# Performance work log

Hardware: AMD Instinct MI355X
Metric: run time of the kernel (lower is better)

## Reference

```python
import jax, jax.numpy as jnp
import numpy as np
import itertools

N = 65536          # points
R = 1.0 / 16.0     # radius (forward uses 1/16)
K = 64             # max_num_neighbors in forward call
G = 16             # grid cells per axis (cell size == R)


def _radius_knn_edges(pts):
    """Grid-hashed radius search; per point keep nearest K within R (self-loop included),
    pad with self index so every point has exactly K edges (max-aggregation neutral)."""
    cells = np.minimum((pts / R).astype(np.int64), G - 1)
    cid = (cells[:, 0] * G + cells[:, 1]) * G + cells[:, 2]
    order = np.argsort(cid, kind='stable')
    sorted_cid = cid[order]
    counts = np.bincount(cid, minlength=G ** 3)
    starts = np.concatenate([[0], np.cumsum(counts)[:-1]])
    M = int(counts.max())
    cand = -np.ones((G ** 3, M), dtype=np.int64)
    slot = np.arange(N) - starts[sorted_cid]
    cand[sorted_cid, slot] = order
    offs = np.array(list(itertools.product([-1, 0, 1], repeat=3)))
    nbr = np.empty((N, K), dtype=np.int64)
    chunk = 4096
    for s in range(0, N, chunk):
        e = min(s + chunk, N)
        c = cells[s:e]
        nc = c[:, None, :] + offs[None]                      # [B,27,3]
        valid_c = np.all((nc >= 0) & (nc < G), axis=-1)      # [B,27]
        ncid = (nc[..., 0] * G + nc[..., 1]) * G + nc[..., 2]
        ncid = np.where(valid_c, ncid, 0)
        cd = cand[ncid]                                      # [B,27,M]
        cd = np.where(np.broadcast_to(valid_c[..., None], cd.shape), cd, -1)
        cd = cd.reshape(e - s, -1)                           # [B,27M]
        p = pts[np.maximum(cd, 0)]
        d = np.linalg.norm(p - pts[s:e, None, :], axis=-1)
        d = np.where((cd >= 0) & (d <= R), d, np.inf)
        sel = np.argsort(d, axis=1)[:, :K]
        row = np.arange(e - s)[:, None]
        picked = cd[row, sel]
        ok = np.isfinite(d[row, sel])
        nbr[s:e] = np.where(ok, picked, np.arange(s, e)[:, None])
    out_index = np.repeat(np.arange(N, dtype=np.int64), K)
    in_index = nbr.reshape(-1)
    return out_index, in_index


def setup_inputs() -> dict:
    key = jax.random.key(0)
    ks = jax.random.split(key, 16)
    pos = jax.random.uniform(ks[0], (N, 3), dtype=jnp.float32)
    rgb = jax.random.uniform(ks[1], (N, 3), dtype=jnp.float32)
    batch = jnp.zeros((N,), dtype=jnp.int64)
    oi, ii = _radius_knn_edges(np.asarray(pos, dtype=np.float64))
    out_index = jnp.asarray(oi)
    in_index = jnp.asarray(ii)

    def lin_w(k, fi, fo):
        return jax.random.normal(k, (fi, fo), dtype=jnp.float32) / np.sqrt(fi).astype(np.float32)

    def lin_b(k, fo):
        return 0.01 * jax.random.normal(k, (fo,), dtype=jnp.float32)

    return {
        'pos': pos, 'rgb': rgb, 'batch': batch,
        'out_index': out_index, 'in_index': in_index,
        'w1a': lin_w(ks[2], 6, 8),   'b1a': lin_b(ks[3], 8),
        'w1b': lin_w(ks[4], 8, 8),   'b1b': lin_b(ks[5], 8),
        'w2a': lin_w(ks[6], 11, 16), 'b2a': lin_b(ks[7], 16),
        'w2b': lin_w(ks[8], 16, 16), 'b2b': lin_b(ks[9], 16),
        'w3a': lin_w(ks[10], 19, 32), 'b3a': lin_b(ks[11], 32),
        'w3b': lin_w(ks[12], 32, 32), 'b3b': lin_b(ks[13], 32),
    }


def _point_conv(x, pos, out_index, in_index, wa, ba, wb, bb):
    # gather neighbor features + relative position, local MLP, max-scatter, output linear
    dpos = pos[in_index] - pos[out_index]                      # [E,3]
    msg = jnp.concatenate([x[in_index], dpos], axis=-1)        # [E,c_in+3]
    h = jax.nn.celu(msg @ wa + ba)                             # [E,c_mid]
    agg = jax.ops.segment_max(h, out_index, num_segments=pos.shape[0],
                              indices_are_sorted=True)         # [N,c_mid]
    return agg @ wb + bb                                       # [N,c_out]


def reference(pos, rgb, batch, out_index, in_index,
              w1a, b1a, w1b, b1b, w2a, b2a, w2b, b2b, w3a, b3a, w3b, b3b):
    out = jax.nn.celu(_point_conv(pos, pos, out_index, in_index, w1a, b1a, w1b, b1b))
    out = jax.nn.celu(_point_conv(out, pos, out_index, in_index, w2a, b2a, w2b, b2b))
    out = jax.nn.celu(_point_conv(out, pos, out_index, in_index, w3a, b3a, w3b, b3b))
    return (pos, out, batch)
```

## Files before the change

kernel.cpp:

```cpp
#include <hip/hip_runtime.h>
#include <hip/hip_fp16.h>
#include <math.h>


#define NPTS 65536
#define KNBR 64

__device__ __forceinline__ float celu1(float x) {
    return x > 0.0f ? x : (__expf(x) - 1.0f);
}

__device__ __forceinline__ unsigned pkmax(unsigned a, unsigned b) {
    unsigned d;
    asm("v_pk_max_f16 %0, %1, %2" : "=v"(d) : "v"(a), "v"(b));
    return d;
}

__device__ __forceinline__ unsigned pack2(float a, float b) {
    __half2 h = __floats2half2_rn(a, b);
    return *(unsigned*)&h;
}

__global__ __launch_bounds__(256) void k_prep(
    const float* __restrict__ pos,
    const float* __restrict__ w1a,
    const float* __restrict__ b1a,
    __half* __restrict__ q1,
    float* __restrict__ dout,
    int out_size)
{
    int t = blockIdx.x * 256 + threadIdx.x;
    if (t >= NPTS) return;
    float p0 = pos[3 * t + 0];
    float p1 = pos[3 * t + 1];
    float p2 = pos[3 * t + 2];
    dout[3 * t + 0] = p0;
    dout[3 * t + 1] = p1;
    dout[3 * t + 2] = p2;
    float q[8];
#pragma unroll
    for (int c = 0; c < 8; ++c) {
        float a = b1a[c];
        a = fmaf(p0, w1a[0 * 8 + c] + w1a[3 * 8 + c], a);
        a = fmaf(p1, w1a[1 * 8 + c] + w1a[4 * 8 + c], a);
        a = fmaf(p2, w1a[2 * 8 + c] + w1a[5 * 8 + c], a);
        q[c] = a;
    }
    uint4 pk;
    pk.x = pack2(q[0], q[1]);
    pk.y = pack2(q[2], q[3]);
    pk.z = pack2(q[4], q[5]);
    pk.w = pack2(q[6], q[7]);
    *(uint4*)(q1 + 8 * t) = pk;
    for (int j = 35 * NPTS + t; j < out_size; j += NPTS)
        dout[j] = 0.0f;
}

template <int FH, int FOUT, int FHN, bool WRITEX>
__global__ __launch_bounds__(256) void k_layer(
    const __half* __restrict__ q,
    const int* __restrict__ idx,
    const float* __restrict__ pos,
    const float* __restrict__ wap,
    const float* __restrict__ wb,
    const float* __restrict__ bb,
    const float* __restrict__ wan,
    const float* __restrict__ ban,
    float* __restrict__ xout,
    __half* __restrict__ qnext)
{
    constexpr int SL  = FH / 8;
    constexpr int LPP = SL * 8;
    constexpr int PPW = 64 / LPP;
    constexpr int NIT = 64 / (4 * PPW);

    __shared__ uint4 m_lds[64 * SL];

    int w  = threadIdx.x >> 6;
    int l  = threadIdx.x & 63;
    int pl = l / LPP;
    int u  = l % LPP;
    int c  = u % SL;
    int g  = u / SL;
    int pbase = blockIdx.x * 64;

#pragma unroll
    for (int it = 0; it < NIT; ++it) {
        int lp = it * (4 * PPW) + w * PPW + pl;
        int p  = pbase + lp;
        const uint4* ip = (const uint4*)(idx + p * KNBR + g * 8);
        uint4 i0 = ip[0];
        uint4 i1 = ip[1];
        uint4 v[8];
        v[0] = *(const uint4*)(q + (int)i0.x * FH + c * 8);
        v[1] = *(const uint4*)(q + (int)i0.y * FH + c * 8);
        v[2] = *(const uint4*)(q + (int)i0.z * FH + c * 8);
        v[3] = *(const uint4*)(q + (int)i0.w * FH + c * 8);
        v[4] = *(const uint4*)(q + (int)i1.x * FH + c * 8);
        v[5] = *(const uint4*)(q + (int)i1.y * FH + c * 8);
        v[6] = *(const uint4*)(q + (int)i1.z * FH + c * 8);
        v[7] = *(const uint4*)(q + (int)i1.w * FH + c * 8);

        unsigned ax = 0xFC00FC00u, ay = 0xFC00FC00u, az = 0xFC00FC00u, aw = 0xFC00FC00u;
#pragma unroll
        for (int k = 0; k < 8; ++k) {
            ax = pkmax(ax, v[k].x);
            ay = pkmax(ay, v[k].y);
            az = pkmax(az, v[k].z);
            aw = pkmax(aw, v[k].w);
        }
#pragma unroll
        for (int st = SL; st < LPP; st <<= 1) {
            ax = pkmax(ax, (unsigned)__shfl_xor((int)ax, st, 64));
            ay = pkmax(ay, (unsigned)__shfl_xor((int)ay, st, 64));
            az = pkmax(az, (unsigned)__shfl_xor((int)az, st, 64));
            aw = pkmax(aw, (unsigned)__shfl_xor((int)aw, st, 64));
        }
        if (g == 0) {
            uint4 r; r.x = ax; r.y = ay; r.z = az; r.w = aw;
            m_lds[lp * SL + c] = r;
        }
    }
    __syncthreads();

    if (threadIdx.x < 64) {
        int lt = threadIdx.x;
        int p  = pbase + lt;
        float p0 = pos[3 * p + 0];
        float p1 = pos[3 * p + 1];
        float p2 = pos[3 * p + 2];

        float h[FH];
#pragma unroll
        for (int s = 0; s < SL; ++s) {
            uint4 vv = m_lds[lt * SL + s];
            unsigned w4[4] = {vv.x, vv.y, vv.z, vv.w};
#pragma unroll
            for (int k = 0; k < 4; ++k) {
                float2 f = __half22float2(*(__half2*)&w4[k]);
                h[s * 8 + k * 2 + 0] = f.x;
                h[s * 8 + k * 2 + 1] = f.y;
            }
        }
#pragma unroll
        for (int ch = 0; ch < FH; ++ch) {
            float gg = p0 * wap[ch] + p1 * wap[FH + ch] + p2 * wap[2 * FH + ch];
            h[ch] = celu1(h[ch] - gg);
        }
        float x[FOUT];
#pragma unroll
        for (int c2 = 0; c2 < FOUT; ++c2) {
            float a = bb[c2];
#pragma unroll
            for (int ch = 0; ch < FH; ++ch)
                a = fmaf(h[ch], wb[ch * FOUT + c2], a);
            x[c2] = celu1(a);
        }
        if constexpr (WRITEX) {
            float4* xo = (float4*)(xout + (long long)p * FOUT);
#pragma unroll
            for (int c4 = 0; c4 < FOUT / 4; ++c4)
                xo[c4] = make_float4(x[4 * c4 + 0], x[4 * c4 + 1], x[4 * c4 + 2], x[4 * c4 + 3]);
        }
        if constexpr (FHN > 0) {
            float qn[FHN];
#pragma unroll
            for (int cn = 0; cn < FHN; ++cn) {
                float a = ban[cn];
#pragma unroll
                for (int c2 = 0; c2 < FOUT; ++c2)
                    a = fmaf(x[c2], wan[c2 * FHN + cn], a);
                a = fmaf(p0, wan[(FOUT + 0) * FHN + cn], a);
                a = fmaf(p1, wan[(FOUT + 1) * FHN + cn], a);
                a = fmaf(p2, wan[(FOUT + 2) * FHN + cn], a);
                qn[cn] = a;
            }
            uint4* qo = (uint4*)(qnext + p * FHN);
#pragma unroll
            for (int s = 0; s < FHN / 8; ++s) {
                uint4 pk;
                pk.x = pack2(qn[s * 8 + 0], qn[s * 8 + 1]);
                pk.y = pack2(qn[s * 8 + 2], qn[s * 8 + 3]);
                pk.z = pack2(qn[s * 8 + 4], qn[s * 8 + 5]);
                pk.w = pack2(qn[s * 8 + 6], qn[s * 8 + 7]);
                qo[s] = pk;
            }
        }
    }
}

extern "C" void kernel_launch(void* const* d_in, const int* in_sizes, int n_in,
                              void* d_out, int out_size, void* d_ws, size_t ws_size,
                              hipStream_t stream) {
    const float* pos = (const float*)d_in[0];
    const int* idx = (const int*)d_in[4];
    const float* w1a = (const float*)d_in[5];
    const float* b1a = (const float*)d_in[6];
    const float* w1b = (const float*)d_in[7];
    const float* b1b = (const float*)d_in[8];
    const float* w2a = (const float*)d_in[9];
    const float* b2a = (const float*)d_in[10];
    const float* w2b = (const float*)d_in[11];
    const float* b2b = (const float*)d_in[12];
    const float* w3a = (const float*)d_in[13];
    const float* b3a = (const float*)d_in[14];
    const float* w3b = (const float*)d_in[15];
    const float* b3b = (const float*)d_in[16];
    float* out = (float*)d_out;

    char* ws = (char*)d_ws;
    __half* A = (__half*)ws;
    __half* B = (__half*)(ws + (4u << 20));

    k_prep<<<NPTS / 256, 256, 0, stream>>>(pos, w1a, b1a, A, out, out_size);
    k_layer<8, 8, 16, false><<<NPTS / 64, 256, 0, stream>>>(
        A, idx, pos, w1a + 3 * 8, w1b, b1b, w2a, b2a, nullptr, B);
    k_layer<16, 16, 32, false><<<NPTS / 64, 256, 0, stream>>>(
        B, idx, pos, w2a + 8 * 16, w2b, b2b, w3a, b3a, nullptr, A);
    k_layer<32, 32, 0, true><<<NPTS / 64, 256, 0, stream>>>(
        A, idx, pos, w3a + 16 * 32, w3b, b3b, nullptr, nullptr, out + 3 * NPTS, nullptr);
}
```

Measured before the change: 177.0 us.

## Fuse prep and three layers into one cooperative persistent kernel with grid syncs

Merges the prep kernel and the three layer kernels into a single cooperative kernel that loops over tiles persistently and separates stages with grid-wide syncs, so the separate launches and the gaps between them go away. The final layer's output MLP is spread across all 256 threads (4 threads per point, 8 outputs each) instead of only 64. The next-layer projection is also computed in chunks of 8 to reduce register pressure. This adds grid-sync cost and a fixed grid of 1024 or 512 blocks, which may limit occupancy compared with the original many-block launches. A fallback to the old multi-kernel path remains.

```diff
diff --git a/kernel.cpp b/kernel.cpp
--- a/kernel.cpp
+++ b/kernel.cpp
@@ -1,10 +1,13 @@
 #include <hip/hip_runtime.h>
 #include <hip/hip_fp16.h>
+#include <hip/hip_cooperative_groups.h>
 #include <math.h>
 
 
 #define NPTS 65536
 #define KNBR 64
+
+namespace cg = cooperative_groups;
 
 __device__ __forceinline__ float celu1(float x) {
     return x > 0.0f ? x : (__expf(x) - 1.0f);
@@ -21,43 +24,9 @@
     return *(unsigned*)&h;
 }
 
-__global__ __launch_bounds__(256) void k_prep(
-    const float* __restrict__ pos,
-    const float* __restrict__ w1a,
-    const float* __restrict__ b1a,
-    __half* __restrict__ q1,
-    float* __restrict__ dout,
-    int out_size)
-{
-    int t = blockIdx.x * 256 + threadIdx.x;
-    if (t >= NPTS) return;
-    float p0 = pos[3 * t + 0];
-    float p1 = pos[3 * t + 1];
-    float p2 = pos[3 * t + 2];
-    dout[3 * t + 0] = p0;
-    dout[3 * t + 1] = p1;
-    dout[3 * t + 2] = p2;
-    float q[8];
-#pragma unroll
-    for (int c = 0; c < 8; ++c) {
-        float a = b1a[c];
-        a = fmaf(p0, w1a[0 * 8 + c] + w1a[3 * 8 + c], a);
-        a = fmaf(p1, w1a[1 * 8 + c] + w1a[4 * 8 + c], a);
-        a = fmaf(p2, w1a[2 * 8 + c] + w1a[5 * 8 + c], a);
-        q[c] = a;
-    }
-    uint4 pk;
-    pk.x = pack2(q[0], q[1]);
-    pk.y = pack2(q[2], q[3]);
-    pk.z = pack2(q[4], q[5]);
-    pk.w = pack2(q[6], q[7]);
-    *(uint4*)(q1 + 8 * t) = pk;
-    for (int j = 35 * NPTS + t; j < out_size; j += NPTS)
-        dout[j] = 0.0f;
-}
-
 template <int FH, int FOUT, int FHN, bool WRITEX>
-__global__ __launch_bounds__(256) void k_layer(
+__device__ __forceinline__ void layer_phase(
+    uint4* __restrict__ m_lds,
     const __half* __restrict__ q,
     const int* __restrict__ idx,
     const float* __restrict__ pos,
@@ -67,14 +36,13 @@
     const float* __restrict__ wan,
     const float* __restrict__ ban,
     float* __restrict__ xout,
-    __half* __restrict__ qnext)
+    __half* __restrict__ qnext,
+    int pbase)
 {
     constexpr int SL  = FH / 8;
     constexpr int LPP = SL * 8;
     constexpr int PPW = 64 / LPP;
     constexpr int NIT = 64 / (4 * PPW);
-
-    __shared__ uint4 m_lds[64 * SL];
 
     int w  = threadIdx.x >> 6;
     int l  = threadIdx.x & 63;
@@ -82,7 +50,6 @@
     int u  = l % LPP;
     int c  = u % SL;
     int g  = u / SL;
-    int pbase = blockIdx.x * 64;
 
 #pragma unroll
     for (int it = 0; it < NIT; ++it) {
@@ -123,7 +90,45 @@
     }
     __syncthreads();
 
-    if (threadIdx.x < 64) {
+    if constexpr (WRITEX) {
+        int pt  = threadIdx.x >> 2;
+        int qtr = threadIdx.x & 3;
+        int p   = pbase + pt;
+        float p0 = pos[3 * p + 0];
+        float p1 = pos[3 * p + 1];
+        float p2 = pos[3 * p + 2];
+
+        float h[FH];
+#pragma unroll
+        for (int s = 0; s < SL; ++s) {
+            uint4 vv = m_lds[pt * SL + s];
+            unsigned w4[4] = {vv.x, vv.y, vv.z, vv.w};
+#pragma unroll
+            for (int k = 0; k < 4; ++k) {
+                float2 f = __half22float2(*(__half2*)&w4[k]);
+                h[s * 8 + k * 2 + 0] = f.x;
+                h[s * 8 + k * 2 + 1] = f.y;
+            }
+        }
+#pragma unroll
+        for (int ch = 0; ch < FH; ++ch) {
+            float gg = p0 * wap[ch] + p1 * wap[FH + ch] + p2 * wap[2 * FH + ch];
+            h[ch] = celu1(h[ch] - gg);
+        }
+        float x[8];
+#pragma unroll
+        for (int j = 0; j < 8; ++j) {
+            int c2 = qtr * 8 + j;
+            float a = bb[c2];
+#pragma unroll
+            for (int ch = 0; ch < FH; ++ch)
+                a = fmaf(h[ch], wb[ch * FOUT + c2], a);
+            x[j] = celu1(a);
+        }
+        float4* xo = (float4*)(xout + (long long)p * FOUT + qtr * 8);
+        xo[0] = make_float4(x[0], x[1], x[2], x[3]);
+        xo[1] = make_float4(x[4], x[5], x[6], x[7]);
+    } else if (threadIdx.x < 64) {
         int lt = threadIdx.x;
         int p  = pbase + lt;
         float p0 = pos[3 * p + 0];
@@ -156,37 +161,129 @@
                 a = fmaf(h[ch], wb[ch * FOUT + c2], a);
             x[c2] = celu1(a);
         }
-        if constexpr (WRITEX) {
-            float4* xo = (float4*)(xout + (long long)p * FOUT);
-#pragma unroll
-            for (int c4 = 0; c4 < FOUT / 4; ++c4)
-                xo[c4] = make_float4(x[4 * c4 + 0], x[4 * c4 + 1], x[4 * c4 + 2], x[4 * c4 + 3]);
-        }
         if constexpr (FHN > 0) {
-            float qn[FHN];
-#pragma unroll
-            for (int cn = 0; cn < FHN; ++cn) {
-                float a = ban[cn];
-#pragma unroll
-                for (int c2 = 0; c2 < FOUT; ++c2)
-                    a = fmaf(x[c2], wan[c2 * FHN + cn], a);
-                a = fmaf(p0, wan[(FOUT + 0) * FHN + cn], a);
-                a = fmaf(p1, wan[(FOUT + 1) * FHN + cn], a);
-                a = fmaf(p2, wan[(FOUT + 2) * FHN + cn], a);
-                qn[cn] = a;
-            }
             uint4* qo = (uint4*)(qnext + p * FHN);
 #pragma unroll
             for (int s = 0; s < FHN / 8; ++s) {
+                float qn[8];
+#pragma unroll
+                for (int k = 0; k < 8; ++k) {
+                    int cn = s * 8 + k;
+                    float a = ban[cn];
+#pragma unroll
+                    for (int c2 = 0; c2 < FOUT; ++c2)
+                        a = fmaf(x[c2], wan[c2 * FHN + cn], a);
+                    a = fmaf(p0, wan[(FOUT + 0) * FHN + cn], a);
+                    a = fmaf(p1, wan[(FOUT + 1) * FHN + cn], a);
+                    a = fmaf(p2, wan[(FOUT + 2) * FHN + cn], a);
+                    qn[k] = a;
+                }
                 uint4 pk;
-                pk.x = pack2(qn[s * 8 + 0], qn[s * 8 + 1]);
-                pk.y = pack2(qn[s * 8 + 2], qn[s * 8 + 3]);
-                pk.z = pack2(qn[s * 8 + 4], qn[s * 8 + 5]);
-                pk.w = pack2(qn[s * 8 + 6], qn[s * 8 + 7]);
+                pk.x = pack2(qn[0], qn[1]);
+                pk.y = pack2(qn[2], qn[3]);
+                pk.z = pack2(qn[4], qn[5]);
+                pk.w = pack2(qn[6], qn[7]);
                 qo[s] = pk;
             }
         }
     }
+    __syncthreads();
+}
+
+__device__ __forceinline__ void prep_body(
+    int t, const float* __restrict__ pos,
+    const float* __restrict__ w1a, const float* __restrict__ b1a,
+    __half* __restrict__ q1, float* __restrict__ dout)
+{
+    float p0 = pos[3 * t + 0];
+    float p1 = pos[3 * t + 1];
+    float p2 = pos[3 * t + 2];
+    dout[3 * t + 0] = p0;
+    dout[3 * t + 1] = p1;
+    dout[3 * t + 2] = p2;
+    float qv[8];
+#pragma unroll
+    for (int c = 0; c < 8; ++c) {
+        float a = b1a[c];
+        a = fmaf(p0, w1a[0 * 8 + c] + w1a[3 * 8 + c], a);
+        a = fmaf(p1, w1a[1 * 8 + c] + w1a[4 * 8 + c], a);
+        a = fmaf(p2, w1a[2 * 8 + c] + w1a[5 * 8 + c], a);
+        qv[c] = a;
+    }
+    uint4 pk;
+    pk.x = pack2(qv[0], qv[1]);
+    pk.y = pack2(qv[2], qv[3]);
+    pk.z = pack2(qv[4], qv[5]);
+    pk.w = pack2(qv[6], qv[7]);
+    *(uint4*)(q1 + 8 * t) = pk;
+}
+
+__global__ __launch_bounds__(256, 4) void k_mega(
+    const float* __restrict__ pos,
+    const int* __restrict__ idx,
+    const float* __restrict__ w1a, const float* __restrict__ b1a,
+    const float* __restrict__ w1b, const float* __restrict__ b1b,
+    const float* __restrict__ w2a, const float* __restrict__ b2a,
+    const float* __restrict__ w2b, const float* __restrict__ b2b,
+    const float* __restrict__ w3a, const float* __restrict__ b3a,
+    const float* __restrict__ w3b, const float* __restrict__ b3b,
+    __half* __restrict__ A, __half* __restrict__ B,
+    float* __restrict__ out, int out_size)
+{
+    __shared__ uint4 m_lds[64 * 4];
+    cg::grid_group grid = cg::this_grid();
+    const int ntiles = NPTS / 64;
+    const int gstride = gridDim.x * 256;
+    int t0 = blockIdx.x * 256 + threadIdx.x;
+
+    for (int t = t0; t < NPTS; t += gstride)
+        prep_body(t, pos, w1a, b1a, A, out);
+    for (int j = 35 * NPTS + t0; j < out_size; j += gstride)
+        out[j] = 0.0f;
+    grid.sync();
+
+    for (int tb = blockIdx.x; tb < ntiles; tb += gridDim.x)
+        layer_phase<8, 8, 16, false>(m_lds, A, idx, pos,
+                                     w1a + 3 * 8, w1b, b1b, w2a, b2a,
+                                     nullptr, B, tb * 64);
+    grid.sync();
+
+    for (int tb = blockIdx.x; tb < ntiles; tb += gridDim.x)
+        layer_phase<16, 16, 32, false>(m_lds, B, idx, pos,
+                                       w2a + 8 * 16, w2b, b2b, w3a, b3a,
+                                       nullptr, A, tb * 64);
+    grid.sync();
+
+    for (int tb = blockIdx.x; tb < ntiles; tb += gridDim.x)
+        layer_phase<32, 32, 0, true>(m_lds, A, idx, pos,
+                                     w3a + 16 * 32, w3b, b3b, nullptr, nullptr,
+                                     out + 3 * NPTS, nullptr, tb * 64);
+}
+
+__global__ __launch_bounds__(256) void k_prep(
+    const float* __restrict__ pos,
+    const float* __restrict__ w1a, const float* __restrict__ b1a,
+    __half* __restrict__ q1, float* __restrict__ dout, int out_size)
+{
+    int t = blockIdx.x * 256 + threadIdx.x;
+    if (t < NPTS)
+        prep_body(t, pos, w1a, b1a, q1, dout);
+    for (int j = 35 * NPTS + t; j < out_size; j += NPTS)
+        dout[j] = 0.0f;
+}
+
+template <int FH, int FOUT, int FHN, bool WRITEX>
+__global__ __launch_bounds__(256) void k_layer(
+    const __half* __restrict__ q, const int* __restrict__ idx,
+    const float* __restrict__ pos,
+    const float* __restrict__ wap, const float* __restrict__ wb,
+    const float* __restrict__ bb,
+    const float* __restrict__ wan, const float* __restrict__ ban,
+    float* __restrict__ xout, __half* __restrict__ qnext)
+{
+    __shared__ uint4 m_lds[64 * 4];
+    layer_phase<FH, FOUT, FHN, WRITEX>(m_lds, q, idx, pos, wap, wb, bb,
+                                       wan, ban, xout, qnext, blockIdx.x * 64);
 }
 
 extern "C" void kernel_launch(void* const* d_in, const int* in_sizes, int n_in,
@@ -212,11 +309,41 @@
     __half* A = (__half*)ws;
     __half* B = (__half*)(ws + (4u << 20));
 
-    k_prep<<<NPTS / 256, 256, 0, stream>>>(pos, w1a, b1a, A, out, out_size);
-    k_layer<8, 8, 16, false><<<NPTS / 64, 256, 0, stream>>>(
-        A, idx, pos, w1a + 3 * 8, w1b, b1b, w2a, b2a, nullptr, B);
-    k_layer<16, 16, 32, false><<<NPTS / 64, 256, 0, stream>>>(
-        B, idx, pos, w2a + 8 * 16, w2b, b2b, w3a, b3a, nullptr, A);
-    k_layer<32, 32, 0, true><<<NPTS / 64, 256, 0, stream>>>(
-        A, idx, pos, w3a + 16 * 32, w3b, b3b, nullptr, nullptr, out + 3 * NPTS, nullptr);
-}
+    static int g_mode = -1;
+    bool launched = false;
+
+    if (g_mode != 0) {
+        void* args[] = {
+            (void*)&pos, (void*)&idx,
+            (void*)&w1a, (void*)&b1a, (void*)&w1b, (void*)&b1b,
+            (void*)&w2a, (void*)&b2a, (void*)&w2b, (void*)&b2b,
+            (void*)&w3a, (void*)&b3a, (void*)&w3b, (void*)&b3b,
+            (void*)&A, (void*)&B, (void*)&out, (void*)&out_size
+        };
+        if (g_mode == -1 || g_mode == 2) {
+            hipError_t e = hipLaunchCooperativeKernel((const void*)k_mega,
+                                                      dim3(1024), dim3(256),
+                                                      args, 0, stream);
+            if (e == hipSuccess) { g_mode = 2; launched = true; }
+            else { (void)hipGetLastError(); if (g_mode == -1) g_mode = 1; else g_mode = 0; }
+        }
+        if (!launched && g_mode == 1) {
+            hipError_t e = hipLaunchCooperativeKernel((const void*)k_mega,
+                                                      dim3(512), dim3(256),
+                                                      args, 0, stream);
+            if (e == hipSuccess) { launched = true; }
+            else { (void)hipGetLastError(); g_mode = 0; }
+        }
+    }
+
+    if (!launched) {
+        k_prep<<<NPTS / 256, 256, 0, stream>>>(pos, w1a, b1a, A, out, out_size);
+        k_layer<8, 8, 16, false><<<NPTS / 64, 256, 0, stream>>>(
+            A, idx, pos, w1a + 3 * 8, w1b, b1b, w2a, b2a, nullptr, B);
+        k_layer<16, 16, 32, false><<<NPTS / 64, 256, 0, stream>>>(
+            B, idx, pos, w2a + 8 * 16, w2b, b2b, w3a, b3a, nullptr, A);
+        k_layer<32, 32, 0, true><<<NPTS / 64, 256, 0, stream>>>(
+            A, idx, pos, w3a + 16 * 32, w3b, b3b, nullptr, nullptr,
+            out + 3 * NPTS, nullptr);
+    }
+}
```

Result: slower. 373.0 us (+110.8%).

## Halve per-block point tile and split final-layer epilogue across four lanes

Applied to the files above, without the earlier changes.

Each block now handles 32 points instead of 64, which doubles the grid and shortens the serial epilogue that only a few lanes run. In the last layer, four threads share each point's 32 output channels instead of one thread doing all of them, spreading the dense MLP work over more lanes. The next-layer projection is computed in 8-channel chunks to cut register pressure, and launch bounds now request 8 blocks per multiprocessor. In exchange there are more blocks and barriers, the h-unpack is repeated by all four lanes of a point, and the gather phase does fewer iterations per block.

```diff
diff --git a/kernel.cpp b/kernel.cpp
--- a/kernel.cpp
+++ b/kernel.cpp
@@ -5,6 +5,7 @@
 
 #define NPTS 65536
 #define KNBR 64
+#define TILE 32
 
 __device__ __forceinline__ float celu1(float x) {
     return x > 0.0f ? x : (__expf(x) - 1.0f);
@@ -57,7 +58,7 @@
 }
 
 template <int FH, int FOUT, int FHN, bool WRITEX>
-__global__ __launch_bounds__(256) void k_layer(
+__global__ __launch_bounds__(256, 8) void k_layer(
     const __half* __restrict__ q,
     const int* __restrict__ idx,
     const float* __restrict__ pos,
@@ -72,9 +73,9 @@
     constexpr int SL  = FH / 8;
     constexpr int LPP = SL * 8;
     constexpr int PPW = 64 / LPP;
-    constexpr int NIT = 64 / (4 * PPW);
-
-    __shared__ uint4 m_lds[64 * SL];
+    constexpr int NIT = TILE / (4 * PPW);
+
+    __shared__ uint4 m_lds[TILE * SL];
 
     int w  = threadIdx.x >> 6;
     int l  = threadIdx.x & 63;
@@ -82,7 +83,7 @@
     int u  = l % LPP;
     int c  = u % SL;
     int g  = u / SL;
-    int pbase = blockIdx.x * 64;
+    int pbase = blockIdx.x * TILE;
 
 #pragma unroll
     for (int it = 0; it < NIT; ++it) {
@@ -123,7 +124,47 @@
     }
     __syncthreads();
 
-    if (threadIdx.x < 64) {
+    if constexpr (WRITEX) {
+        if (threadIdx.x < TILE * 4) {
+            int pt  = threadIdx.x >> 2;
+            int qtr = threadIdx.x & 3;
+            int p   = pbase + pt;
+            float p0 = pos[3 * p + 0];
+            float p1 = pos[3 * p + 1];
+            float p2 = pos[3 * p + 2];
+
+            float h[FH];
+#pragma unroll
+            for (int s = 0; s < SL; ++s) {
+                uint4 vv = m_lds[pt * SL + s];
+                unsigned w4[4] = {vv.x, vv.y, vv.z, vv.w};
+#pragma unroll
+                for (int k = 0; k < 4; ++k) {
+                    float2 f = __half22float2(*(__half2*)&w4[k]);
+                    h[s * 8 + k * 2 + 0] = f.x;
+                    h[s * 8 + k * 2 + 1] = f.y;
+                }
+            }
+#pragma unroll
+            for (int ch = 0; ch < FH; ++ch) {
+                float gg = p0 * wap[ch] + p1 * wap[FH + ch] + p2 * wap[2 * FH + ch];
+                h[ch] = celu1(h[ch] - gg);
+            }
+            float x[8];
+#pragma unroll
+            for (int j = 0; j < 8; ++j) {
+                int c2 = qtr * 8 + j;
+                float a = bb[c2];
+#pragma unroll
+                for (int ch = 0; ch < FH; ++ch)
+                    a = fmaf(h[ch], wb[ch * FOUT + c2], a);
+                x[j] = celu1(a);
+            }
+            float4* xo = (float4*)(xout + (long long)p * FOUT + qtr * 8);
+            xo[0] = make_float4(x[0], x[1], x[2], x[3]);
+            xo[1] = make_float4(x[4], x[5], x[6], x[7]);
+        }
+    } else if (threadIdx.x < TILE) {
         int lt = threadIdx.x;
         int p  = pbase + lt;
         float p0 = pos[3 * p + 0];
@@ -156,33 +197,28 @@
                 a = fmaf(h[ch], wb[ch * FOUT + c2], a);
             x[c2] = celu1(a);
         }
-        if constexpr (WRITEX) {
-            float4* xo = (float4*)(xout + (long long)p * FOUT);
-#pragma unroll
-            for (int c4 = 0; c4 < FOUT / 4; ++c4)
-                xo[c4] = make_float4(x[4 * c4 + 0], x[4 * c4 + 1], x[4 * c4 + 2], x[4 * c4 + 3]);
-        }
         if constexpr (FHN > 0) {
-            float qn[FHN];
-#pragma unroll
-            for (int cn = 0; cn < FHN; ++cn) {
-                float a = ban[cn];
-#pragma unroll
-                for (int c2 = 0; c2 < FOUT; ++c2)
-                    a = fmaf(x[c2], wan[c2 * FHN + cn], a);
-                a = fmaf(p0, wan[(FOUT + 0) * FHN + cn], a);
-                a = fmaf(p1, wan[(FOUT + 1) * FHN + cn], a);
-                a = fmaf(p2, wan[(FOUT + 2) * FHN + cn], a);
-                qn[cn] = a;
-            }
             uint4* qo = (uint4*)(qnext + p * FHN);
 #pragma unroll
             for (int s = 0; s < FHN / 8; ++s) {
+                float qn[8];
+#pragma unroll
+                for (int k = 0; k < 8; ++k) {
+                    int cn = s * 8 + k;
+                    float a = ban[cn];
+#pragma unroll
+                    for (int c2 = 0; c2 < FOUT; ++c2)
+                        a = fmaf(x[c2], wan[c2 * FHN + cn], a);
+                    a = fmaf(p0, wan[(FOUT + 0) * FHN + cn], a);
+                    a = fmaf(p1, wan[(FOUT + 1) * FHN + cn], a);
+                    a = fmaf(p2, wan[(FOUT + 2) * FHN + cn], a);
+                    qn[k] = a;
+                }
                 uint4 pk;
-                pk.x = pack2(qn[s * 8 + 0], qn[s * 8 + 1]);
-                pk.y = pack2(qn[s * 8 + 2], qn[s * 8 + 3]);
-                pk.z = pack2(qn[s * 8 + 4], qn[s * 8 + 5]);
-                pk.w = pack2(qn[s * 8 + 6], qn[s * 8 + 7]);
+                pk.x = pack2(qn[0], qn[1]);
+                pk.y = pack2(qn[2], qn[3]);
+                pk.z = pack2(qn[4], qn[5]);
+                pk.w = pack2(qn[6], qn[7]);
                 qo[s] = pk;
             }
         }
@@ -213,10 +249,10 @@
     __half* B = (__half*)(ws + (4u << 20));
 
     k_prep<<<NPTS / 256, 256, 0, stream>>>(pos, w1a, b1a, A, out, out_size);
-    k_layer<8, 8, 16, false><<<NPTS / 64, 256, 0, stream>>>(
+    k_layer<8, 8, 16, false><<<NPTS / TILE, 256, 0, stream>>>(
         A, idx, pos, w1a + 3 * 8, w1b, b1b, w2a, b2a, nullptr, B);
-    k_layer<16, 16, 32, false><<<NPTS / 64, 256, 0, stream>>>(
+    k_layer<16, 16, 32, false><<<NPTS / TILE, 256, 0, stream>>>(
         B, idx, pos, w2a + 8 * 16, w2b, b2b, w3a, b3a, nullptr, A);
-    k_layer<32, 32, 0, true><<<NPTS / 64, 256, 0, stream>>>(
+    k_layer<32, 32, 0, true><<<NPTS / TILE, 256, 0, stream>>>(
         A, idx, pos, w3a + 16 * 32, w3b, b3b, nullptr, nullptr, out + 3 * NPTS, nullptr);
 }
```

Result: no change. 178.0 us (+0.6%).
